# Performance work log

Measured on AMD Instinct MI355X. Metric: run time of the kernel, lower is better.

Reference implementation:

```python
import jax, jax.numpy as jnp
import numpy as np

B, T, X, H, Z, Y, G = 4096, 32, 256, 256, 128, 2, 128


def setup_inputs() -> dict:
    key = jax.random.key(0)
    ks = jax.random.split(key, 16)
    rn = lambda k, s, sc=0.05: jax.random.normal(k, s, dtype=jnp.float32) * sc
    n_days = jnp.concatenate([jnp.array([T], dtype=jnp.int32),
                              jax.random.randint(ks[2], (B - 1,), 1, T + 1).astype(jnp.int32)])
    return {
        "x": rn(ks[0], (B, T, X), 1.0),
        "y_true": jax.nn.softmax(jax.random.normal(ks[1], (B, T, Y), dtype=jnp.float32), axis=-1),
        "n_days": n_days,
        "z0": rn(ks[3], (B, Z), 1.0),
        "eps": rn(ks[4], (T, B, Z), 1.0),
        "W_ih": rn(ks[5], (3 * H, X)), "W_hh": rn(ks[6], (3 * H, H)),
        "b_ih": jnp.zeros((3 * H,), jnp.float32), "b_hh": jnp.zeros((3 * H,), jnp.float32),
        "Wph": rn(ks[7], (Z, X + H + Z)), "bph": jnp.zeros((Z,), jnp.float32),
        "Woh": rn(ks[8], (Z, X + H + Y + Z)), "boh": jnp.zeros((Z,), jnp.float32),
        "Wpm": rn(ks[9], (Z, Z)), "bpm": jnp.zeros((Z,), jnp.float32),
        "Wps": rn(ks[10], (Z, Z)), "bps": jnp.zeros((Z,), jnp.float32),
        "Wqm": rn(ks[11], (Z, Z)), "bqm": jnp.zeros((Z,), jnp.float32),
        "Wqs": rn(ks[12], (Z, Z)), "bqs": jnp.zeros((Z,), jnp.float32),
        "Wg": rn(ks[13], (G, H + Z)), "bg": jnp.zeros((G,), jnp.float32),
        "Wy": rn(ks[14], (Y, G)), "by": jnp.zeros((Y,), jnp.float32),
    }


def _forward(x, y_true, z0, eps, W_ih, W_hh, b_ih, b_hh, Wph, bph, Woh, boh,
             Wpm, bpm, Wps, bps, Wqm, bqm, Wqs, bqs, Wg, bg, Wy, by, n_days):
    xt = jnp.transpose(x, (1, 0, 2))       # [T, B, X]
    yt = jnp.transpose(y_true, (1, 0, 2))  # [T, B, Y]

    # --- GRU over time (torch nn.GRU gate math) ---
    def gru_step(h, xi):
        gi = xi @ W_ih.T + b_ih
        gh = h @ W_hh.T + b_hh
        ir, iz, inn = jnp.split(gi, 3, axis=-1)
        hr, hz, hn = jnp.split(gh, 3, axis=-1)
        r = jax.nn.sigmoid(ir + hr)
        u = jax.nn.sigmoid(iz + hz)
        n = jnp.tanh(inn + r * hn)
        h_new = (1.0 - u) * n + u * h
        return h_new, h_new

    h0 = jnp.zeros((x.shape[0], H), x.dtype)
    _, hs = jax.lax.scan(gru_step, h0, xt)  # [T, B, H]
    # pack/pad semantics: padded timesteps produce zero outputs
    valid = jnp.arange(T)[:, None] < n_days[None, :]  # [T, B]
    hs = jnp.where(valid[:, :, None], hs, 0.0)

    # --- sequential VAE latent scan: z_t depends on z_{t-1} ---
    def vmd_step(z, inputs):
        xi, hi, yi, ei = inputs
        hzp = jnp.tanh(jnp.concatenate([xi, hi, z], -1) @ Wph.T + bph)
        mp = hzp @ Wpm.T + bpm
        sp = jnp.sqrt(jnp.exp(hzp @ Wps.T + bps))
        hzq = jnp.tanh(jnp.concatenate([xi, hi, yi, z], -1) @ Woh.T + boh)
        mq = hzq @ Wqm.T + bqm
        sq = jnp.sqrt(jnp.exp(hzq @ Wqs.T + bqs))
        z_post = mq + sq * ei
        # kl_normal_normal(post || prior)
        kl = jnp.log(sp / sq) + (sq * sq + (mq - mp) ** 2) / (2.0 * sp * sp) - 0.5
        return z_post, (z_post, kl)

    _, (z_posts, kls_e) = jax.lax.scan(vmd_step, z0, (xt, hs, yt, eps))
    kls = jnp.sum(kls_e, axis=-1).T  # [B, T]

    hz = jnp.concatenate([jnp.transpose(hs, (1, 0, 2)),
                          jnp.transpose(z_posts, (1, 0, 2))], -1)  # [B, T, H+Z]
    g = jnp.tanh(hz @ Wg.T + bg)                     # [B, T, G]
    y_pred = jax.nn.softmax(g @ Wy.T + by, axis=-1)  # [B, T, Y]

    idx = n_days - 1
    b = jnp.arange(x.shape[0])
    g_T = g[b, idx]       # [B, G]
    y_T = y_pred[b, idx]  # [B, Y]
    return jnp.concatenate([g_T, y_T, kls], axis=-1)  # [B, G+Y+T]


def reference(x, y_true, n_days, z0, eps, W_ih, W_hh, b_ih, b_hh, Wph, bph,
              Woh, boh, Wpm, bpm, Wps, bps, Wqm, bqm, Wqs, bqs, Wg, bg, Wy, by):
    return _forward(x, y_true, z0, eps, W_ih, W_hh, b_ih, b_hh, Wph, bph, Woh,
                    boh, Wpm, bpm, Wps, bps, Wqm, bqm, Wqs, bqs, Wg, bg, Wy, by,
                    n_days)
```

## Files before the change

kernel.cpp:

```cpp
#include <hip/hip_runtime.h>

typedef unsigned short u16;
typedef short bf16x8 __attribute__((ext_vector_type(8)));
typedef float f32x4 __attribute__((ext_vector_type(4)));

__device__ __forceinline__ float bf2f(u16 v){
  union { unsigned u; float f; } x; x.u = ((unsigned)v) << 16; return x.f;
}
__device__ __forceinline__ u16 f2bf(float f){
  union { float f; unsigned u; } x; x.f = f;
  unsigned u = x.u;
  u += 0x7fffu + ((u >> 16) & 1u);
  return (u16)(u >> 16);
}
__device__ __forceinline__ unsigned pk_bf16(float lo, float hi){
  unsigned r;
  asm("v_cvt_pk_bf16_f32 %0, %1, %2" : "=v"(r) : "v"(lo), "v"(hi));
  return r;
}
__device__ __forceinline__ u16 el4(ushort4 v, int r){ return r==0?v.x:r==1?v.y:r==2?v.z:v.w; }
__device__ __forceinline__ float elf4(float4 v, int r){ return r==0?v.x:r==1?v.y:r==2?v.z:v.w; }
__device__ __forceinline__ float sigm(float x){ return 1.f/(1.f+__expf(-x)); }
__device__ __forceinline__ float tanh_s(float x){ return 1.f - 2.f/(__expf(2.f*x)+1.f); }
__device__ __forceinline__ f32x4 mfma16(bf16x8 a, bf16x8 b, f32x4 c){
  return __builtin_amdgcn_mfma_f32_16x16x32_bf16(a, b, c, 0, 0, 0);
}
__device__ __forceinline__ void gl2lds16(const void* g, void* l){
  __builtin_amdgcn_global_load_lds(
      (const __attribute__((address_space(1))) unsigned int*)g,
      (__attribute__((address_space(3))) unsigned int*)l, 16, 0, 0);
}

__global__ void prep_w(const float* __restrict__ W_ih, const float* __restrict__ W_hh,
                       const float* __restrict__ Wph, const float* __restrict__ Woh,
                       const float* __restrict__ Wpm, const float* __restrict__ Wps,
                       const float* __restrict__ Wqm, const float* __restrict__ Wqs,
                       const float* __restrict__ Wg,  const float* __restrict__ bph,
                       const float* __restrict__ boh,
                       u16* __restrict__ wsb, float* __restrict__ Woy, float* __restrict__ bpq)
{
  int idx = blockIdx.x*256 + threadIdx.x;
  if (idx < 196608){ wsb[idx] = f2bf(W_ih[idx]); return; }
  if (idx < 393216){ wsb[idx] = f2bf(W_hh[idx-196608]); return; }
  if (idx < 524288){ int j = idx-393216; int row = j>>9, col = j&511;
    float v = (row<128) ? Wph[row*640+col] : Woh[(row-128)*642+col];
    wsb[idx] = f2bf(v); return; }
  if (idx < 540672){ int j = idx-524288; int row=j>>7, col=j&127; wsb[idx]=f2bf(Wph[row*640+512+col]); return; }
  if (idx < 557056){ int j = idx-540672; int row=j>>7, col=j&127; wsb[idx]=f2bf(Woh[row*642+514+col]); return; }
  if (idx < 573440){ wsb[idx]=f2bf(Wpm[idx-557056]); return; }
  if (idx < 589824){ wsb[idx]=f2bf(Wps[idx-573440]); return; }
  if (idx < 606208){ wsb[idx]=f2bf(Wqm[idx-589824]); return; }
  if (idx < 622592){ wsb[idx]=f2bf(Wqs[idx-606208]); return; }
  if (idx < 671744){ wsb[idx]=f2bf(Wg[idx-622592]); return; }
  if (idx < 672000){ int j = idx-671744; int row=j>>1; Woy[j] = Woh[row*642+512+(j&1)]; return; }
  if (idx < 672256){ int j = idx-672000; bpq[j] = (j<128) ? bph[j] : boh[j-128]; return; }
}

__global__ void prep_b(const float* __restrict__ b_ih, const float* __restrict__ b_hh,
                       float* __restrict__ bsum)
{
  int j = threadIdx.x;
  if (j < 768) bsum[j] = b_ih[j] + (j < 512 ? b_hh[j] : 0.f);
}

__global__ void prep_x(const float* __restrict__ x, u16* __restrict__ xbf){
  int i = blockIdx.x*256 + threadIdx.x;
  if (i >= 4194304) return;
  const float4* src = (const float4*)(x + (size_t)i*8);
  float4 a = src[0], b = src[1];
  uint4 o;
  o.x = pk_bf16(a.x, a.y);
  o.y = pk_bf16(a.z, a.w);
  o.z = pk_bf16(b.x, b.y);
  o.w = pk_bf16(b.z, b.w);
  ((uint4*)xbf)[i] = o;
}

__global__ void sort_days(const int* __restrict__ n_days, int* __restrict__ perm,
                          int* __restrict__ nd_s, int* __restrict__ cnt)
{
  __shared__ int hist[34];
  __shared__ int base[34];
  __shared__ int cursor[34];
  int tid = threadIdx.x;
  if (tid < 34) hist[tid] = 0;
  __syncthreads();
  for (int i = tid; i < 4096; i += 1024) atomicAdd(&hist[n_days[i]], 1);
  __syncthreads();
  if (tid == 0){
    int acc = 0;
    for (int v = 32; v >= 1; --v){ base[v] = acc; acc += hist[v]; }
    base[0] = acc;
  }
  __syncthreads();
  if (tid < 33) cursor[tid] = base[tid];
  if (tid < 32) cnt[tid] = base[tid];
  __syncthreads();
  for (int i = tid; i < 4096; i += 1024){
    int v = n_days[i];
    int pos = atomicAdd(&cursor[v], 1);
    perm[pos] = i;
    nd_s[pos] = v;
  }
}

__global__ __launch_bounds__(512, 4) void gemm_gi(
  const u16* __restrict__ A, const u16* __restrict__ W,
  const float* __restrict__ bias, const int* __restrict__ perm,
  const int* __restrict__ cnt, u16* __restrict__ C)
{
  const int t  = blockIdx.x >> 5;
  const int rt = blockIdx.x & 31;
  if (rt*128 >= cnt[t]) return;
  const int n0 = blockIdx.y*256;
  const int tid = threadIdx.x;
  const int w = tid>>6, lane = tid&63, c = lane&15, g = lane>>4;
  const int wm = w>>2, wn = w&3;
  __shared__ __align__(16) char smem[49152];
  u16* abuf = (u16*)smem;
  u16* wbuf = (u16*)(smem + 16384);
  u16* clds = (u16*)smem;

  size_t asrc[2];
  #pragma unroll
  for (int i=0;i<2;++i){
    int p = (w*2+i)*64 + lane;
    int k8 = p>>7, row = p&127;
    asrc[i] = ((size_t)perm[rt*128 + row]*32 + t)*256 + k8*8;
  }
  size_t wsrc[4];
  #pragma unroll
  for (int i=0;i<4;++i){
    int p = (w*4+i)*64 + lane;
    int k8 = p>>8, row = p&255;
    wsrc[i] = (size_t)(n0+row)*256 + k8*8;
  }
  f32x4 acc[4][4];
  #pragma unroll
  for (int i=0;i<4;++i)
    #pragma unroll
    for (int j=0;j<4;++j) acc[i][j] = (f32x4){0.f,0.f,0.f,0.f};
  for (int kc=0; kc<4; ++kc){
    __syncthreads();
    #pragma unroll
    for (int i=0;i<2;++i) gl2lds16(A + asrc[i] + kc*64, &abuf[(w*2+i)*512]);
    #pragma unroll
    for (int i=0;i<4;++i) gl2lds16(W + wsrc[i] + kc*64, &wbuf[(w*4+i)*512]);
    __syncthreads();
    #pragma unroll
    for (int ks=0;ks<2;++ks){
      int k8 = ks*4 + g;
      bf16x8 a[4];
      #pragma unroll
      for (int mt=0;mt<4;++mt) a[mt] = *(const bf16x8*)&abuf[(k8*128 + wm*64 + mt*16 + c)*8];
      #pragma unroll
      for (int nt=0;nt<4;++nt){
        bf16x8 b = *(const bf16x8*)&wbuf[(k8*256 + wn*64 + nt*16 + c)*8];
        #pragma unroll
        for (int mt=0;mt<4;++mt)
          acc[mt][nt] = mfma16(a[mt], b, acc[mt][nt]);
      }
    }
  }
  __syncthreads();
  const size_t crow = (size_t)t*4096 + rt*128;
  #pragma unroll
  for (int nh=0; nh<2; ++nh){
    if ((wn>>1) == nh){
      #pragma unroll
      for (int nt=0;nt<4;++nt){
        int n = n0 + wn*64 + nt*16 + c;
        float bn = bias[n];
        int lc = (wn&1)*64 + nt*16 + c;
        #pragma unroll
        for (int mt=0;mt<4;++mt){
          int lr = wm*64 + mt*16 + g*4;
          #pragma unroll
          for (int r=0;r<4;++r)
            clds[(lr+r)*136 + lc] = f2bf(acc[mt][nt][r] + bn);
        }
      }
    }
    __syncthreads();
    #pragma unroll
    for (int p=0;p<4;++p){
      int idx = p*512 + tid;
      int row = idx>>4, ch = idx&15;
      *(uint4*)(C + (crow+row)*768 + n0 + nh*128 + ch*8)
        = *(const uint4*)&clds[row*136 + ch*8];
    }
    __syncthreads();
  }
}

__global__ __launch_bounds__(512, 4) void gemm_hpq(
  const u16* __restrict__ A1, const u16* __restrict__ A2,
  const u16* __restrict__ W, const float* __restrict__ bias,
  const float* __restrict__ yt, const float* __restrict__ Woy,
  u16* __restrict__ C)
{
  const int m0 = blockIdx.x*128;
  const int tid = threadIdx.x;
  const int w = tid>>6, lane = tid&63, c = lane&15, g = lane>>4;
  const int wm = w>>2, wn = w&3;
  __shared__ __align__(16) char smem[49152];
  u16* abuf = (u16*)smem;
  u16* wbuf = (u16*)(smem + 16384);
  u16* clds = (u16*)smem;

  size_t asrc[2];
  #pragma unroll
  for (int i=0;i<2;++i){
    int p = (w*2+i)*64 + lane;
    int k8 = p>>7, row = p&127;
    asrc[i] = (size_t)(m0+row)*256 + k8*8;
  }
  size_t wsrc[4];
  #pragma unroll
  for (int i=0;i<4;++i){
    int p = (w*4+i)*64 + lane;
    int k8 = p>>8, row = p&255;
    wsrc[i] = (size_t)row*512 + k8*8;
  }
  f32x4 acc[4][4];
  #pragma unroll
  for (int i=0;i<4;++i)
    #pragma unroll
    for (int j=0;j<4;++j) acc[i][j] = (f32x4){0.f,0.f,0.f,0.f};
  for (int kc=0; kc<8; ++kc){
    __syncthreads();
    const u16* Ab = (kc < 4) ? A1 : A2;
    int ko = (kc & 3)*64;
    #pragma unroll
    for (int i=0;i<2;++i) gl2lds16(Ab + asrc[i] + ko, &abuf[(w*2+i)*512]);
    #pragma unroll
    for (int i=0;i<4;++i) gl2lds16(W + wsrc[i] + kc*64, &wbuf[(w*4+i)*512]);
    __syncthreads();
    #pragma unroll
    for (int ks=0;ks<2;++ks){
      int k8 = ks*4 + g;
      bf16x8 a[4];
      #pragma unroll
      for (int mt=0;mt<4;++mt) a[mt] = *(const bf16x8*)&abuf[(k8*128 + wm*64 + mt*16 + c)*8];
      #pragma unroll
      for (int nt=0;nt<4;++nt){
        bf16x8 b = *(const bf16x8*)&wbuf[(k8*256 + wn*64 + nt*16 + c)*8];
        #pragma unroll
        for (int mt=0;mt<4;++mt)
          acc[mt][nt] = mfma16(a[mt], b, acc[mt][nt]);
      }
    }
  }
  __syncthreads();
  #pragma unroll
  for (int nh=0; nh<2; ++nh){
    if ((wn>>1) == nh){
      #pragma unroll
      for (int nt=0;nt<4;++nt){
        int n = wn*64 + nt*16 + c;
        float bn = bias[n];
        float wy0 = 0.f, wy1 = 0.f;
        bool yfl = (n >= 128);
        if (yfl){ wy0 = Woy[(n-128)*2]; wy1 = Woy[(n-128)*2+1]; }
        int lc = (wn&1)*64 + nt*16 + c;
        #pragma unroll
        for (int mt=0;mt<4;++mt){
          int lr = wm*64 + mt*16 + g*4;
          #pragma unroll
          for (int r=0;r<4;++r){
            size_t m = (size_t)m0 + lr + r;
            float v = acc[mt][nt][r] + bn;
            if (yfl) v += yt[2*m]*wy0 + yt[2*m+1]*wy1;
            clds[(lr+r)*136 + lc] = f2bf(v);
          }
        }
      }
    }
    __syncthreads();
    #pragma unroll
    for (int p=0;p<4;++p){
      int idx = p*512 + tid;
      int row = idx>>4, ch = idx&15;
      *(uint4*)(C + (size_t)(m0+row)*256 + nh*128 + ch*8)
        = *(const uint4*)&clds[row*136 + ch*8];
    }
    __syncthreads();
  }
}

__global__ __launch_bounds__(1024, 4) void gru_seq(
  const u16* __restrict__ GI, const u16* __restrict__ Whh,
  const float* __restrict__ bhh, const int* __restrict__ perm,
  const int* __restrict__ nd_s, u16* __restrict__ hs)
{
  const int b0 = blockIdx.x*16;
  const int tid = threadIdx.x;
  const int w = tid>>6, lane = tid&63, c = lane&15, g = lane>>4;
  const int j0 = w*16 + g*4;
  __shared__ __align__(16) u16 hbuf[2][4096];
  __shared__ __align__(16) u16 gibuf[5][12288];

  bf16x8 wa[3][8];
  #pragma unroll
  for (int gate=0; gate<3; ++gate)
    #pragma unroll
    for (int ks=0; ks<8; ++ks)
      wa[gate][ks] = *(const bf16x8*)&Whh[(size_t)(gate*256 + w*16 + c)*256 + ks*32 + g*8];

  const float4 bhn4 = *(const float4*)(bhh + 512 + j0);
  const int ndc   = nd_s[b0 + c];
  const int bound = nd_s[b0];
  const int ob    = perm[b0 + c];

  int so0, so1;
  { int pe = w*512 + lane*8; int row = pe/768, off = pe - row*768;
    so0 = (b0+row)*768 + (off ^ ((row&7)<<3)); }
  { int pe = (16+w)*512 + lane*8; int row = pe/768, off = pe - row*768;
    so1 = (b0+row)*768 + (off ^ ((row&7)<<3)); }
  const int rd0 = c*1536 + ((j0*2) ^ ((c&7)<<4));
  const int hroff = (g*16 + c)*16;
  const int hwoff = ((w*2 + (g>>1))*16 + c)*16 + (g&1)*8;
  u16* hsp = hs + (size_t)ob*8192 + j0;

  float hprev[4] = {0.f,0.f,0.f,0.f};
  if (tid < 512) ((uint4*)hbuf[0])[tid] = make_uint4(0,0,0,0);

  const size_t PL = 3145728;
  #pragma unroll
  for (int p=0; p<4; ++p){
    int pp = (p < bound) ? p : bound-1;
    gl2lds16(GI + (size_t)pp*PL + so0, (char*)gibuf[p] + w*1024);
    if (w < 8) gl2lds16(GI + (size_t)pp*PL + so1, (char*)gibuf[p] + (16+w)*1024);
  }
  asm volatile("s_waitcnt vmcnt(0)" ::: "memory");
  __syncthreads();

  const u16* hr = hbuf[0];
  u16*       hw = hbuf[1];
  int cur = 0;
  #pragma unroll 1
  for (int t=0; t<bound; ++t){
    if (w < 8) asm volatile("s_waitcnt vmcnt(9)" ::: "memory");
    else       asm volatile("s_waitcnt vmcnt(6)" ::: "memory");
    __builtin_amdgcn_sched_barrier(0);
    const char* gib = (const char*)gibuf[cur];
    ushort4 gr_ = *(const ushort4*)(gib + rd0);
    ushort4 gu_ = *(const ushort4*)(gib + rd0 + 512);
    ushort4 gn_ = *(const ushort4*)(gib + rd0 + 1024);
    f32x4 aR = (f32x4){0.f,0.f,0.f,0.f};
    f32x4 aU = (f32x4){0.f,0.f,0.f,0.f};
    f32x4 aN = (f32x4){bhn4.x, bhn4.y, bhn4.z, bhn4.w};
    __builtin_amdgcn_s_setprio(1);
    #pragma unroll
    for (int ks=0; ks<8; ++ks){
      bf16x8 hf = *(const bf16x8*)((const char*)hr + hroff + ks*1024);
      aR = mfma16(wa[0][ks], hf, aR);
      aU = mfma16(wa[1][ks], hf, aU);
      aN = mfma16(wa[2][ks], hf, aN);
    }
    __builtin_amdgcn_s_setprio(0);
    {
      float h4[4];
      #pragma unroll
      for (int r=0; r<4; ++r){
        float rr = sigm(bf2f(el4(gr_,r)) + aR[r]);
        float uu = sigm(bf2f(el4(gu_,r)) + aU[r]);
        float nn = tanh_s(bf2f(el4(gn_,r)) + rr*aN[r]);
        float h = nn + uu*(hprev[r]-nn);
        hprev[r] = h;
        h4[r] = h;
      }
      uint2 hpk;
      hpk.x = pk_bf16(h4[0], h4[1]);
      hpk.y = pk_bf16(h4[2], h4[3]);
      *(uint2*)((char*)hw + hwoff) = hpk;
      uint2 hst = (t < ndc) ? hpk : make_uint2(0u,0u);
      *(uint2*)(hsp + t*256) = hst;
    }
    __builtin_amdgcn_sched_barrier(0);
    {
      int pf = (t+4 < bound) ? t+4 : bound-1;
      int nxt = cur;
      nxt = cur >= 1 ? cur-1 : 4;
      gl2lds16(GI + (size_t)pf*PL + so0, (char*)gibuf[nxt] + w*1024);
      if (w < 8) gl2lds16(GI + (size_t)pf*PL + so1, (char*)gibuf[nxt] + (16+w)*1024);
    }
    asm volatile("s_waitcnt lgkmcnt(0)" ::: "memory");
    __builtin_amdgcn_sched_barrier(0);
    __builtin_amdgcn_s_barrier();
    __builtin_amdgcn_sched_barrier(0);
    { const u16* tmp = hr; hr = hw; hw = (u16*)tmp; }
    cur = (cur == 4) ? 0 : cur+1;
  }
  for (int t2 = bound; t2 < 32; ++t2)
    *(uint2*)(hsp + t2*256) = make_uint2(0u,0u);
}

__global__ __launch_bounds__(512) void vae_seq(
  const u16* __restrict__ HPQ, const float* __restrict__ z0,
  const float* __restrict__ eps, const int* __restrict__ n_days,
  const u16* __restrict__ Wm,
  const float* __restrict__ bpm, const float* __restrict__ bps,
  const float* __restrict__ bqm, const float* __restrict__ bqs,
  u16* __restrict__ zidx, float* __restrict__ out)
{
  const int b0 = blockIdx.x*16;
  const int tid = threadIdx.x, w = tid>>6, lane = tid&63, c = lane&15;
  const int g2 = lane>>4;
  const int j0 = w*16 + g2*4;
  __shared__ __align__(16) u16 zbuf[16*16*8];
  __shared__ __align__(16) u16 hzpb[16*16*8];
  __shared__ __align__(16) u16 hzqb[16*16*8];
  __shared__ float klb[32][16][8];

  bf16x8 wf[6][4];
  #pragma unroll
  for (int mat=0;mat<6;++mat)
    #pragma unroll
    for (int ks=0;ks<4;++ks)
      wf[mat][ks] = *(const bf16x8*)&Wm[mat*16384 + (w*16+c)*128 + ks*32 + g2*8];

  const float4 bpm4 = *(const float4*)(bpm + j0);
  const float4 bps4 = *(const float4*)(bps + j0);
  const float4 bqm4 = *(const float4*)(bqm + j0);
  const float4 bqs4 = *(const float4*)(bqs + j0);
  const int ndc = n_days[b0 + c];

  const int hroff = (g2*16 + c)*16;
  const int hwoff = ((w*2 + (g2>>1))*16 + c)*16 + (g2&1)*8;
  const u16*  hbp = HPQ + ((size_t)(b0+c)*32)*256 + j0;
  const float* ebp = eps + (size_t)(b0+c)*128 + j0;

  if (tid < 256){
    int k8 = tid>>4, row = tid&15;
    const float* zp = z0 + (size_t)(b0+row)*128 + k8*8;
    uint4 o;
    o.x = pk_bf16(zp[0], zp[1]);
    o.y = pk_bf16(zp[2], zp[3]);
    o.z = pk_bf16(zp[4], zp[5]);
    o.w = pk_bf16(zp[6], zp[7]);
    ((uint4*)zbuf)[tid] = o;
  }
  __syncthreads();

  ushort4 pA = *(const ushort4*)(hbp);
  ushort4 qA = *(const ushort4*)(hbp + 128);
  float4  eA = *(const float4*)(ebp);
  ushort4 pB = *(const ushort4*)(hbp + 256);
  ushort4 qB = *(const ushort4*)(hbp + 384);
  float4  eB = *(const float4*)(ebp + 524288);

  uint2 zsel = make_uint2(0u,0u);

  auto step = [&](ushort4& hp4, ushort4& hq4, float4& e4, int t){
    f32x4 accP = (f32x4){0,0,0,0}, accQ = (f32x4){0,0,0,0};
    #pragma unroll
    for (int ks=0;ks<4;++ks){
      bf16x8 zf = *(const bf16x8*)((const char*)zbuf + hroff + ks*1024);
      accP = mfma16(wf[0][ks], zf, accP);
      accQ = mfma16(wf[1][ks], zf, accQ);
    }
    float p4[4], q4[4];
    #pragma unroll
    for (int r=0;r<4;++r){
      p4[r] = tanh_s(bf2f(el4(hp4,r)) + accP[r]);
      q4[r] = tanh_s(bf2f(el4(hq4,r)) + accQ[r]);
    }
    uint2 ppk, qpk;
    ppk.x = pk_bf16(p4[0], p4[1]);  ppk.y = pk_bf16(p4[2], p4[3]);
    qpk.x = pk_bf16(q4[0], q4[1]);  qpk.y = pk_bf16(q4[2], q4[3]);
    *(uint2*)((char*)hzpb + hwoff) = ppk;
    *(uint2*)((char*)hzqb + hwoff) = qpk;
    asm volatile("s_waitcnt lgkmcnt(0)" ::: "memory");
    __builtin_amdgcn_sched_barrier(0);
    __builtin_amdgcn_s_barrier();
    __builtin_amdgcn_sched_barrier(0);
    f32x4 aMP=(f32x4){0,0,0,0}, aAP=(f32x4){0,0,0,0};
    f32x4 aMQ=(f32x4){0,0,0,0}, aAQ=(f32x4){0,0,0,0};
    #pragma unroll
    for (int ks=0;ks<4;++ks){
      bf16x8 pf = *(const bf16x8*)((const char*)hzpb + hroff + ks*1024);
      bf16x8 qf = *(const bf16x8*)((const char*)hzqb + hroff + ks*1024);
      aMP = mfma16(wf[2][ks], pf, aMP);
      aAP = mfma16(wf[3][ks], pf, aAP);
      aMQ = mfma16(wf[4][ks], qf, aMQ);
      aAQ = mfma16(wf[5][ks], qf, aAQ);
    }
    float kls = 0.f;
    float z4[4];
    #pragma unroll
    for (int r=0;r<4;++r){
      float mp = aMP[r]+elf4(bpm4,r);
      float ap = aAP[r]+elf4(bps4,r);
      float mq = aMQ[r]+elf4(bqm4,r);
      float aq = aAQ[r]+elf4(bqs4,r);
      float ev = elf4(e4,r);
      float z = mq + __expf(0.5f*aq)*ev;
      float d = mq - mp;
      kls += 0.5f*(ap-aq) + 0.5f*(__expf(aq)+d*d)*__expf(-ap) - 0.5f;
      z4[r] = z;
    }
    uint2 zpk;
    zpk.x = pk_bf16(z4[0], z4[1]);
    zpk.y = pk_bf16(z4[2], z4[3]);
    *(uint2*)((char*)zbuf + hwoff) = zpk;
    if (t == ndc-1) zsel = zpk;
    kls += __shfl_xor(kls, 16);
    kls += __shfl_xor(kls, 32);
    if (lane < 16) klb[t][c][w] = kls;
    if (t < 30){
      hp4 = *(const ushort4*)(hbp + (t+2)*256);
      hq4 = *(const ushort4*)(hbp + (t+2)*256 + 128);
      e4  = *(const float4*)(ebp + (size_t)(t+2)*524288);
    }
    asm volatile("s_waitcnt lgkmcnt(0)" ::: "memory");
    __builtin_amdgcn_sched_barrier(0);
    __builtin_amdgcn_s_barrier();
    __builtin_amdgcn_sched_barrier(0);
  };

  #pragma unroll 1
  for (int t=0; t<32; t+=2){
    step(pA, qA, eA, t);
    step(pB, qB, eB, t+1);
  }

  *(uint2*)(zidx + (size_t)(b0+c)*128 + j0) = zsel;
  {
    int t2 = tid>>4, c2 = tid&15;
    float s = 0.f;
    #pragma unroll
    for (int ww=0;ww<8;++ww) s += klb[t2][c2][ww];
    out[(size_t)(b0+c2)*162 + 130 + t2] = s;
  }
}

__global__ __launch_bounds__(128) void head_k(
  const u16* __restrict__ hs, const u16* __restrict__ zidx,
  const int* __restrict__ n_days, const u16* __restrict__ Wgb,
  const float* __restrict__ bg, const float* __restrict__ Wy,
  const float* __restrict__ by, float* __restrict__ out)
{
  const int b = blockIdx.x;
  const int tid = threadIdx.x;
  const int lane = tid & 63, wv = tid >> 6;
  __shared__ float hz[384];
  __shared__ float red[2][2];
  const int idx = n_days[b]-1;
  const u16* hrow = hs + ((size_t)b*32 + idx)*256;
  for (int k=tid; k<256; k+=128) hz[k] = bf2f(hrow[k]);
  hz[256+tid] = bf2f(zidx[(size_t)b*128 + tid]);
  __syncthreads();
  const u16* wrow = Wgb + (size_t)tid*384;
  float s = 0.f;
  #pragma unroll 4
  for (int k8=0;k8<48;++k8){
    bf16x8 wvv = *(const bf16x8*)&wrow[k8*8];
    #pragma unroll
    for (int e=0;e<8;++e) s += bf2f((u16)wvv[e]) * hz[k8*8+e];
  }
  float gv = tanh_s(s + bg[tid]);
  out[(size_t)b*162 + tid] = gv;
  float a0 = gv*Wy[tid], a1 = gv*Wy[128+tid];
  #pragma unroll
  for (int off=1; off<64; off<<=1){
    a0 += __shfl_xor(a0, off);
    a1 += __shfl_xor(a1, off);
  }
  if (lane == 0){ red[0][wv] = a0; red[1][wv] = a1; }
  __syncthreads();
  if (tid == 0){
    float l0 = by[0] + red[0][0] + red[0][1];
    float l1 = by[1] + red[1][0] + red[1][1];
    float mx = fmaxf(l0,l1);
    float e0 = __expf(l0-mx), e1 = __expf(l1-mx);
    float si = e0+e1;
    out[(size_t)b*162 + 128] = e0/si;
    out[(size_t)b*162 + 129] = e1/si;
  }
}

extern "C" void kernel_launch(void* const* d_in, const int* in_sizes, int n_in,
                              void* d_out, int out_size, void* d_ws, size_t ws_size,
                              hipStream_t stream)
{
  const float* x      = (const float*)d_in[0];
  const float* y_true = (const float*)d_in[1];
  const int*   n_days = (const int*)d_in[2];
  const float* z0     = (const float*)d_in[3];
  const float* eps    = (const float*)d_in[4];
  const float* W_ih   = (const float*)d_in[5];
  const float* W_hh   = (const float*)d_in[6];
  const float* b_ih   = (const float*)d_in[7];
  const float* b_hh   = (const float*)d_in[8];
  const float* Wph    = (const float*)d_in[9];
  const float* bph    = (const float*)d_in[10];
  const float* Woh    = (const float*)d_in[11];
  const float* boh    = (const float*)d_in[12];
  const float* Wpm    = (const float*)d_in[13];
  const float* bpm    = (const float*)d_in[14];
  const float* Wps    = (const float*)d_in[15];
  const float* bps    = (const float*)d_in[16];
  const float* Wqm    = (const float*)d_in[17];
  const float* bqm    = (const float*)d_in[18];
  const float* Wqs    = (const float*)d_in[19];
  const float* bqs    = (const float*)d_in[20];
  const float* Wg     = (const float*)d_in[21];
  const float* bg     = (const float*)d_in[22];
  const float* Wy     = (const float*)d_in[23];
  const float* by     = (const float*)d_in[24];
  (void)in_sizes; (void)n_in; (void)out_size; (void)ws_size;

  u16*   wsb = (u16*)d_ws;
  float* wsf = (float*)d_ws;
  int*   wsi = (int*)d_ws;
  u16* Wih_b = wsb + 0;
  u16* Whh_b = wsb + 196608;
  u16* Wc_b  = wsb + 393216;
  u16* Wz_b  = wsb + 524288;
  u16* Wg_b  = wsb + 622592;
  float* Woy  = wsf + 335872;
  float* bpq  = wsf + 336128;
  float* bsum = wsf + 336384;
  int* perm   = wsi + 337152;
  int* nd_s   = wsi + 341248;
  int* cnt    = wsi + 345344;
  u16* xbf   = wsb + 690752;
  u16* GI    = wsb + 34245184;
  u16* hsB   = wsb + 134908480;
  u16* HPQ   = wsb + 168462912;
  u16* zidx  = wsb + 202017344;

  hipLaunchKernelGGL(prep_w, dim3(2626), dim3(256), 0, stream,
                     W_ih, W_hh, Wph, Woh, Wpm, Wps, Wqm, Wqs, Wg, bph, boh,
                     wsb, Woy, bpq);
  hipLaunchKernelGGL(prep_b, dim3(1), dim3(768), 0, stream, b_ih, b_hh, bsum);
  hipLaunchKernelGGL(prep_x, dim3(16384), dim3(256), 0, stream, x, xbf);
  hipLaunchKernelGGL(sort_days, dim3(1), dim3(1024), 0, stream,
                     n_days, perm, nd_s, cnt);
  hipLaunchKernelGGL(gemm_gi, dim3(1024,3), dim3(512), 0, stream,
                     xbf, Wih_b, bsum, perm, cnt, GI);
  hipLaunchKernelGGL(gru_seq, dim3(256), dim3(1024), 0, stream,
                     GI, Whh_b, b_hh, perm, nd_s, hsB);
  hipLaunchKernelGGL(gemm_hpq, dim3(1024), dim3(512), 0, stream,
                     xbf, hsB, Wc_b, bpq, y_true, Woy, HPQ);
  hipLaunchKernelGGL(vae_seq, dim3(256), dim3(512), 0, stream,
                     HPQ, z0, eps, n_days, Wz_b, bpm, bps, bqm, bqs, zidx, (float*)d_out);
  hipLaunchKernelGGL(head_k, dim3(4096), dim3(128), 0, stream,
                     hsB, zidx, n_days, Wg_b, bg, Wy, by, (float*)d_out);
}
```

Baseline: 489.8 us.

## Halve GRU batch tile to 8 rows and launch twice as many blocks

The sequential GRU kernel now gives each block 8 sorted batch rows instead of 16, so 512 blocks launch instead of 256 and the MI355X's compute units are better filled during the latency-bound recurrence. The MFMA still computes 16 columns, but lanes with c>=8 skip the gate math and stores, and the GI prefetch buffers and load mapping are shrunk to match. In exchange, half of each MFMA's work is wasted, the W_hh fragment loads are duplicated across twice as many blocks, and the __launch_bounds__ change to 8 may tighten register limits.

```diff
diff --git a/kernel.cpp b/kernel.cpp
--- a/kernel.cpp
+++ b/kernel.cpp
@@ -288,17 +288,18 @@
   }
 }
 
-__global__ __launch_bounds__(1024, 4) void gru_seq(
+__global__ __launch_bounds__(1024, 8) void gru_seq(
   const u16* __restrict__ GI, const u16* __restrict__ Whh,
   const float* __restrict__ bhh, const int* __restrict__ perm,
   const int* __restrict__ nd_s, u16* __restrict__ hs)
 {
-  const int b0 = blockIdx.x*16;
+  const int b0 = blockIdx.x*8;
   const int tid = threadIdx.x;
   const int w = tid>>6, lane = tid&63, c = lane&15, g = lane>>4;
   const int j0 = w*16 + g*4;
+  const bool act = (c < 8);
   __shared__ __align__(16) u16 hbuf[2][4096];
-  __shared__ __align__(16) u16 gibuf[5][12288];
+  __shared__ __align__(16) u16 gibuf[5][6144];
 
   bf16x8 wa[3][8];
   #pragma unroll
@@ -308,29 +309,28 @@
       wa[gate][ks] = *(const bf16x8*)&Whh[(size_t)(gate*256 + w*16 + c)*256 + ks*32 + g*8];
 
   const float4 bhn4 = *(const float4*)(bhh + 512 + j0);
-  const int ndc   = nd_s[b0 + c];
   const int bound = nd_s[b0];
-  const int ob    = perm[b0 + c];
-
-  int so0, so1;
-  { int pe = w*512 + lane*8; int row = pe/768, off = pe - row*768;
-    so0 = (b0+row)*768 + (off ^ ((row&7)<<3)); }
-  { int pe = (16+w)*512 + lane*8; int row = pe/768, off = pe - row*768;
-    so1 = (b0+row)*768 + (off ^ ((row&7)<<3)); }
+  const int ndc   = act ? nd_s[b0 + c] : 0;
+  const int ob    = act ? perm[b0 + c] : 0;
+
+  int so;
+  { int pe = w*384 + lane*8;
+    int row = pe/768; if (row > 7) row = 7;
+    int off = pe - row*768; if (off > 760) off = 760;
+    so = (b0+row)*768 + (off ^ ((row&7)<<3)); }
   const int rd0 = c*1536 + ((j0*2) ^ ((c&7)<<4));
   const int hroff = (g*16 + c)*16;
   const int hwoff = ((w*2 + (g>>1))*16 + c)*16 + (g&1)*8;
   u16* hsp = hs + (size_t)ob*8192 + j0;
 
   float hprev[4] = {0.f,0.f,0.f,0.f};
-  if (tid < 512) ((uint4*)hbuf[0])[tid] = make_uint4(0,0,0,0);
+  ((uint4*)hbuf)[tid] = make_uint4(0,0,0,0);
 
   const size_t PL = 3145728;
   #pragma unroll
   for (int p=0; p<4; ++p){
     int pp = (p < bound) ? p : bound-1;
-    gl2lds16(GI + (size_t)pp*PL + so0, (char*)gibuf[p] + w*1024);
-    if (w < 8) gl2lds16(GI + (size_t)pp*PL + so1, (char*)gibuf[p] + (16+w)*1024);
+    if (lane < 48) gl2lds16(GI + (size_t)pp*PL + so, (char*)gibuf[p] + w*768);
   }
   asm volatile("s_waitcnt vmcnt(0)" ::: "memory");
   __syncthreads();
@@ -340,13 +340,8 @@
   int cur = 0;
   #pragma unroll 1
   for (int t=0; t<bound; ++t){
-    if (w < 8) asm volatile("s_waitcnt vmcnt(9)" ::: "memory");
-    else       asm volatile("s_waitcnt vmcnt(6)" ::: "memory");
-    __builtin_amdgcn_sched_barrier(0);
-    const char* gib = (const char*)gibuf[cur];
-    ushort4 gr_ = *(const ushort4*)(gib + rd0);
-    ushort4 gu_ = *(const ushort4*)(gib + rd0 + 512);
-    ushort4 gn_ = *(const ushort4*)(gib + rd0 + 1024);
+    asm volatile("s_waitcnt vmcnt(6)" ::: "memory");
+    __builtin_amdgcn_sched_barrier(0);
     f32x4 aR = (f32x4){0.f,0.f,0.f,0.f};
     f32x4 aU = (f32x4){0.f,0.f,0.f,0.f};
     f32x4 aN = (f32x4){bhn4.x, bhn4.y, bhn4.z, bhn4.w};
@@ -359,7 +354,11 @@
       aN = mfma16(wa[2][ks], hf, aN);
     }
     __builtin_amdgcn_s_setprio(0);
-    {
+    if (act){
+      const char* gib = (const char*)gibuf[cur];
+      ushort4 gr_ = *(const ushort4*)(gib + rd0);
+      ushort4 gu_ = *(const ushort4*)(gib + rd0 + 512);
+      ushort4 gn_ = *(const ushort4*)(gib + rd0 + 1024);
       float h4[4];
       #pragma unroll
       for (int r=0; r<4; ++r){
@@ -380,10 +379,8 @@
     __builtin_amdgcn_sched_barrier(0);
     {
       int pf = (t+4 < bound) ? t+4 : bound-1;
-      int nxt = cur;
-      nxt = cur >= 1 ? cur-1 : 4;
-      gl2lds16(GI + (size_t)pf*PL + so0, (char*)gibuf[nxt] + w*1024);
-      if (w < 8) gl2lds16(GI + (size_t)pf*PL + so1, (char*)gibuf[nxt] + (16+w)*1024);
+      int nxt = cur >= 1 ? cur-1 : 4;
+      if (lane < 48) gl2lds16(GI + (size_t)pf*PL + so, (char*)gibuf[nxt] + w*768);
     }
     asm volatile("s_waitcnt lgkmcnt(0)" ::: "memory");
     __builtin_amdgcn_sched_barrier(0);
@@ -392,8 +389,10 @@
     { const u16* tmp = hr; hr = hw; hw = (u16*)tmp; }
     cur = (cur == 4) ? 0 : cur+1;
   }
-  for (int t2 = bound; t2 < 32; ++t2)
-    *(uint2*)(hsp + t2*256) = make_uint2(0u,0u);
+  if (act){
+    for (int t2 = bound; t2 < 32; ++t2)
+      *(uint2*)(hsp + t2*256) = make_uint2(0u,0u);
+  }
 }
 
 __global__ __launch_bounds__(512) void vae_seq(
@@ -640,7 +639,7 @@
                      n_days, perm, nd_s, cnt);
   hipLaunchKernelGGL(gemm_gi, dim3(1024,3), dim3(512), 0, stream,
                      xbf, Wih_b, bsum, perm, cnt, GI);
-  hipLaunchKernelGGL(gru_seq, dim3(256), dim3(1024), 0, stream,
+  hipLaunchKernelGGL(gru_seq, dim3(512), dim3(1024), 0, stream,
                      GI, Whh_b, b_hh, perm, nd_s, hsB);
   hipLaunchKernelGGL(gemm_hpq, dim3(1024), dim3(512), 0, stream,
                      xbf, hsB, Wc_b, bpq, y_true, Woy, HPQ);
```

Result: slower. 897.9 us (+83.3%).

## Halve GRU recurrence block to 8 waves, each computing two column tiles

Applied to the files above, without the earlier changes.

The sequential GRU kernel now runs 512 threads per block instead of 1024. Each wave owns 32 hidden columns (two 16-wide MFMA tiles), so it holds twice the W_hh fragments in registers and issues six MFMAs per k-step. This is meant to cut barrier cost per timestep and make the GI prefetch uniform across waves (three loads each). In exchange it raises register pressure (48 bf16x8 weight vectors per thread) and gives fewer waves to hide latency on the serial critical path.

```diff
diff --git a/kernel.cpp b/kernel.cpp
--- a/kernel.cpp
+++ b/kernel.cpp
@@ -288,7 +288,7 @@
   }
 }
 
-__global__ __launch_bounds__(1024, 4) void gru_seq(
+__global__ __launch_bounds__(512, 2) void gru_seq(
   const u16* __restrict__ GI, const u16* __restrict__ Whh,
   const float* __restrict__ bhh, const int* __restrict__ perm,
   const int* __restrict__ nd_s, u16* __restrict__ hs)
@@ -296,41 +296,54 @@
   const int b0 = blockIdx.x*16;
   const int tid = threadIdx.x;
   const int w = tid>>6, lane = tid&63, c = lane&15, g = lane>>4;
-  const int j0 = w*16 + g*4;
+  const int j0 = w*32 + g*4;
   __shared__ __align__(16) u16 hbuf[2][4096];
   __shared__ __align__(16) u16 gibuf[5][12288];
-
-  bf16x8 wa[3][8];
+  __shared__ float bhnl[256];
+
+  bf16x8 wa[3][2][8];
   #pragma unroll
   for (int gate=0; gate<3; ++gate)
     #pragma unroll
-    for (int ks=0; ks<8; ++ks)
-      wa[gate][ks] = *(const bf16x8*)&Whh[(size_t)(gate*256 + w*16 + c)*256 + ks*32 + g*8];
-
-  const float4 bhn4 = *(const float4*)(bhh + 512 + j0);
+    for (int ct=0; ct<2; ++ct)
+      #pragma unroll
+      for (int ks=0; ks<8; ++ks)
+        wa[gate][ct][ks] = *(const bf16x8*)&Whh[(size_t)(gate*256 + w*32 + ct*16 + c)*256 + ks*32 + g*8];
+
+  if (tid < 256) bhnl[tid] = bhh[512 + tid];
+  const int bound = nd_s[b0];
   const int ndc   = nd_s[b0 + c];
-  const int bound = nd_s[b0];
   const int ob    = perm[b0 + c];
 
-  int so0, so1;
-  { int pe = w*512 + lane*8; int row = pe/768, off = pe - row*768;
-    so0 = (b0+row)*768 + (off ^ ((row&7)<<3)); }
-  { int pe = (16+w)*512 + lane*8; int row = pe/768, off = pe - row*768;
-    so1 = (b0+row)*768 + (off ^ ((row&7)<<3)); }
-  const int rd0 = c*1536 + ((j0*2) ^ ((c&7)<<4));
+  int so[3];
+  #pragma unroll
+  for (int i=0;i<3;++i){
+    int pe = (w*3+i)*512 + lane*8;
+    int row = pe/768, off = pe - row*768;
+    so[i] = (b0+row)*768 + (off ^ ((row&7)<<3));
+  }
+  const int rdA = c*1536 + ((j0*2) ^ ((c&7)<<4));
+  const int rdB = c*1536 + (((j0+16)*2) ^ ((c&7)<<4));
   const int hroff = (g*16 + c)*16;
-  const int hwoff = ((w*2 + (g>>1))*16 + c)*16 + (g&1)*8;
+  const int hwoffA = ((w*4 + (g>>1))*16 + c)*16 + (g&1)*8;
+  const int hwoffB = hwoffA + 512;
   u16* hsp = hs + (size_t)ob*8192 + j0;
 
-  float hprev[4] = {0.f,0.f,0.f,0.f};
-  if (tid < 512) ((uint4*)hbuf[0])[tid] = make_uint4(0,0,0,0);
+  float hprev[2][4];
+  #pragma unroll
+  for (int ct=0;ct<2;++ct)
+    #pragma unroll
+    for (int r=0;r<4;++r) hprev[ct][r] = 0.f;
+  ((uint4*)hbuf)[tid] = make_uint4(0,0,0,0);
+  ((uint4*)hbuf)[tid+512] = make_uint4(0,0,0,0);
 
   const size_t PL = 3145728;
   #pragma unroll
   for (int p=0; p<4; ++p){
     int pp = (p < bound) ? p : bound-1;
-    gl2lds16(GI + (size_t)pp*PL + so0, (char*)gibuf[p] + w*1024);
-    if (w < 8) gl2lds16(GI + (size_t)pp*PL + so1, (char*)gibuf[p] + (16+w)*1024);
+    #pragma unroll
+    for (int i=0;i<3;++i)
+      gl2lds16(GI + (size_t)pp*PL + so[i], (char*)gibuf[p] + (w*3+i)*1024);
   }
   asm volatile("s_waitcnt vmcnt(0)" ::: "memory");
   __syncthreads();
@@ -340,50 +353,62 @@
   int cur = 0;
   #pragma unroll 1
   for (int t=0; t<bound; ++t){
-    if (w < 8) asm volatile("s_waitcnt vmcnt(9)" ::: "memory");
-    else       asm volatile("s_waitcnt vmcnt(6)" ::: "memory");
-    __builtin_amdgcn_sched_barrier(0);
-    const char* gib = (const char*)gibuf[cur];
-    ushort4 gr_ = *(const ushort4*)(gib + rd0);
-    ushort4 gu_ = *(const ushort4*)(gib + rd0 + 512);
-    ushort4 gn_ = *(const ushort4*)(gib + rd0 + 1024);
-    f32x4 aR = (f32x4){0.f,0.f,0.f,0.f};
-    f32x4 aU = (f32x4){0.f,0.f,0.f,0.f};
-    f32x4 aN = (f32x4){bhn4.x, bhn4.y, bhn4.z, bhn4.w};
+    asm volatile("s_waitcnt vmcnt(15)" ::: "memory");
+    __builtin_amdgcn_sched_barrier(0);
+    float4 bhnA = *(const float4*)&bhnl[j0];
+    float4 bhnB = *(const float4*)&bhnl[j0+16];
+    f32x4 aR0=(f32x4){0,0,0,0}, aR1=(f32x4){0,0,0,0};
+    f32x4 aU0=(f32x4){0,0,0,0}, aU1=(f32x4){0,0,0,0};
+    f32x4 aN0=(f32x4){bhnA.x,bhnA.y,bhnA.z,bhnA.w};
+    f32x4 aN1=(f32x4){bhnB.x,bhnB.y,bhnB.z,bhnB.w};
     __builtin_amdgcn_s_setprio(1);
     #pragma unroll
     for (int ks=0; ks<8; ++ks){
       bf16x8 hf = *(const bf16x8*)((const char*)hr + hroff + ks*1024);
-      aR = mfma16(wa[0][ks], hf, aR);
-      aU = mfma16(wa[1][ks], hf, aU);
-      aN = mfma16(wa[2][ks], hf, aN);
+      aR0 = mfma16(wa[0][0][ks], hf, aR0);
+      aR1 = mfma16(wa[0][1][ks], hf, aR1);
+      aU0 = mfma16(wa[1][0][ks], hf, aU0);
+      aU1 = mfma16(wa[1][1][ks], hf, aU1);
+      aN0 = mfma16(wa[2][0][ks], hf, aN0);
+      aN1 = mfma16(wa[2][1][ks], hf, aN1);
     }
     __builtin_amdgcn_s_setprio(0);
     {
-      float h4[4];
-      #pragma unroll
-      for (int r=0; r<4; ++r){
-        float rr = sigm(bf2f(el4(gr_,r)) + aR[r]);
-        float uu = sigm(bf2f(el4(gu_,r)) + aU[r]);
-        float nn = tanh_s(bf2f(el4(gn_,r)) + rr*aN[r]);
-        float h = nn + uu*(hprev[r]-nn);
-        hprev[r] = h;
-        h4[r] = h;
+      const char* gib = (const char*)gibuf[cur];
+      #pragma unroll
+      for (int ct=0; ct<2; ++ct){
+        int rd = ct ? rdB : rdA;
+        ushort4 gr_ = *(const ushort4*)(gib + rd);
+        ushort4 gu_ = *(const ushort4*)(gib + rd + 512);
+        ushort4 gn_ = *(const ushort4*)(gib + rd + 1024);
+        f32x4 aR = ct ? aR1 : aR0;
+        f32x4 aU = ct ? aU1 : aU0;
+        f32x4 aN = ct ? aN1 : aN0;
+        float h4[4];
+        #pragma unroll
+        for (int r=0; r<4; ++r){
+          float rr = sigm(bf2f(el4(gr_,r)) + aR[r]);
+          float uu = sigm(bf2f(el4(gu_,r)) + aU[r]);
+          float nn = tanh_s(bf2f(el4(gn_,r)) + rr*aN[r]);
+          float h = nn + uu*(hprev[ct][r]-nn);
+          hprev[ct][r] = h;
+          h4[r] = h;
+        }
+        uint2 hpk;
+        hpk.x = pk_bf16(h4[0], h4[1]);
+        hpk.y = pk_bf16(h4[2], h4[3]);
+        *(uint2*)((char*)hw + (ct ? hwoffB : hwoffA)) = hpk;
+        uint2 hst = (t < ndc) ? hpk : make_uint2(0u,0u);
+        *(uint2*)(hsp + t*256 + ct*16) = hst;
       }
-      uint2 hpk;
-      hpk.x = pk_bf16(h4[0], h4[1]);
-      hpk.y = pk_bf16(h4[2], h4[3]);
-      *(uint2*)((char*)hw + hwoff) = hpk;
-      uint2 hst = (t < ndc) ? hpk : make_uint2(0u,0u);
-      *(uint2*)(hsp + t*256) = hst;
     }
     __builtin_amdgcn_sched_barrier(0);
     {
       int pf = (t+4 < bound) ? t+4 : bound-1;
-      int nxt = cur;
-      nxt = cur >= 1 ? cur-1 : 4;
-      gl2lds16(GI + (size_t)pf*PL + so0, (char*)gibuf[nxt] + w*1024);
-      if (w < 8) gl2lds16(GI + (size_t)pf*PL + so1, (char*)gibuf[nxt] + (16+w)*1024);
+      int nxt = cur >= 1 ? cur-1 : 4;
+      #pragma unroll
+      for (int i=0;i<3;++i)
+        gl2lds16(GI + (size_t)pf*PL + so[i], (char*)gibuf[nxt] + (w*3+i)*1024);
     }
     asm volatile("s_waitcnt lgkmcnt(0)" ::: "memory");
     __builtin_amdgcn_sched_barrier(0);
@@ -392,8 +417,10 @@
     { const u16* tmp = hr; hr = hw; hw = (u16*)tmp; }
     cur = (cur == 4) ? 0 : cur+1;
   }
-  for (int t2 = bound; t2 < 32; ++t2)
+  for (int t2 = bound; t2 < 32; ++t2){
     *(uint2*)(hsp + t2*256) = make_uint2(0u,0u);
+    *(uint2*)(hsp + t2*256 + 16) = make_uint2(0u,0u);
+  }
 }
 
 __global__ __launch_bounds__(512) void vae_seq(
@@ -640,7 +667,7 @@
                      n_days, perm, nd_s, cnt);
   hipLaunchKernelGGL(gemm_gi, dim3(1024,3), dim3(512), 0, stream,
                      xbf, Wih_b, bsum, perm, cnt, GI);
-  hipLaunchKernelGGL(gru_seq, dim3(256), dim3(1024), 0, stream,
+  hipLaunchKernelGGL(gru_seq, dim3(256), dim3(512), 0, stream,
                      GI, Whh_b, b_hh, perm, nd_s, hsB);
   hipLaunchKernelGGL(gemm_hpq, dim3(1024), dim3(512), 0, stream,
                      xbf, hsB, Wc_b, bpq, y_true, Woy, HPQ);
```

Result: slower. 507.6 us (+3.6%).

## Rewrite head kernel to batch 16 rows per block using MFMA

Applied to the files above, without the earlier changes.

The output head kernel now handles 16 batch rows per 512-thread block. It stages the selected hidden and latent rows in LDS and computes the Wg projection with bf16 MFMA instructions instead of a per-thread scalar dot product. The Wy logits are then reduced with shuffles, softmaxed, and the g and y outputs are written out cooperatively. This cuts block count and scalar FMA work for a small tail kernel, at the cost of more LDS staging and barriers.

```diff
diff --git a/kernel.cpp b/kernel.cpp
--- a/kernel.cpp
+++ b/kernel.cpp
@@ -380,8 +380,7 @@
     __builtin_amdgcn_sched_barrier(0);
     {
       int pf = (t+4 < bound) ? t+4 : bound-1;
-      int nxt = cur;
-      nxt = cur >= 1 ? cur-1 : 4;
+      int nxt = cur >= 1 ? cur-1 : 4;
       gl2lds16(GI + (size_t)pf*PL + so0, (char*)gibuf[nxt] + w*1024);
       if (w < 8) gl2lds16(GI + (size_t)pf*PL + so1, (char*)gibuf[nxt] + (16+w)*1024);
     }
@@ -535,48 +534,78 @@
   }
 }
 
-__global__ __launch_bounds__(128) void head_k(
+__global__ __launch_bounds__(512) void head_k(
   const u16* __restrict__ hs, const u16* __restrict__ zidx,
   const int* __restrict__ n_days, const u16* __restrict__ Wgb,
   const float* __restrict__ bg, const float* __restrict__ Wy,
   const float* __restrict__ by, float* __restrict__ out)
 {
-  const int b = blockIdx.x;
+  const int b0 = blockIdx.x*16;
   const int tid = threadIdx.x;
-  const int lane = tid & 63, wv = tid >> 6;
-  __shared__ float hz[384];
-  __shared__ float red[2][2];
-  const int idx = n_days[b]-1;
-  const u16* hrow = hs + ((size_t)b*32 + idx)*256;
-  for (int k=tid; k<256; k+=128) hz[k] = bf2f(hrow[k]);
-  hz[256+tid] = bf2f(zidx[(size_t)b*128 + tid]);
-  __syncthreads();
-  const u16* wrow = Wgb + (size_t)tid*384;
-  float s = 0.f;
-  #pragma unroll 4
-  for (int k8=0;k8<48;++k8){
-    bf16x8 wvv = *(const bf16x8*)&wrow[k8*8];
-    #pragma unroll
-    for (int e=0;e<8;++e) s += bf2f((u16)wvv[e]) * hz[k8*8+e];
-  }
-  float gv = tanh_s(s + bg[tid]);
-  out[(size_t)b*162 + tid] = gv;
-  float a0 = gv*Wy[tid], a1 = gv*Wy[128+tid];
-  #pragma unroll
-  for (int off=1; off<64; off<<=1){
-    a0 += __shfl_xor(a0, off);
-    a1 += __shfl_xor(a1, off);
-  }
-  if (lane == 0){ red[0][wv] = a0; red[1][wv] = a1; }
-  __syncthreads();
-  if (tid == 0){
-    float l0 = by[0] + red[0][0] + red[0][1];
-    float l1 = by[1] + red[1][0] + red[1][1];
-    float mx = fmaxf(l0,l1);
-    float e0 = __expf(l0-mx), e1 = __expf(l1-mx);
-    float si = e0+e1;
-    out[(size_t)b*162 + 128] = e0/si;
-    out[(size_t)b*162 + 129] = e1/si;
+  const int w = tid>>6, lane = tid&63, c = lane&15, g = lane>>4;
+  __shared__ __align__(16) u16 hzlds[48*16*8];
+  __shared__ float glds[16*128];
+  __shared__ float ylds[16][2];
+
+  for (int i=tid; i<768; i+=512){
+    int row = i & 15, k8 = i >> 4;
+    int b = b0 + row;
+    uint4 v;
+    if (k8 < 32){
+      int idx = n_days[b] - 1;
+      v = *(const uint4*)(hs + ((size_t)b*32 + idx)*256 + k8*8);
+    } else {
+      v = *(const uint4*)(zidx + (size_t)b*128 + (k8-32)*8);
+    }
+    *(uint4*)&hzlds[((size_t)k8*16 + row)*8] = v;
+  }
+  bf16x8 wf[12];
+  #pragma unroll
+  for (int ks=0;ks<12;++ks)
+    wf[ks] = *(const bf16x8*)&Wgb[(size_t)(w*16 + c)*384 + ks*32 + g*8];
+  const float4 bg4 = *(const float4*)(bg + w*16 + g*4);
+  __syncthreads();
+
+  f32x4 acc = (f32x4){0.f,0.f,0.f,0.f};
+  #pragma unroll
+  for (int ks=0;ks<12;++ks){
+    bf16x8 hzf = *(const bf16x8*)&hzlds[((ks*4+g)*16 + c)*8];
+    acc = mfma16(wf[ks], hzf, acc);
+  }
+  #pragma unroll
+  for (int r=0;r<4;++r){
+    float gv = tanh_s(acc[r] + elf4(bg4,r));
+    glds[c*128 + w*16 + g*4 + r] = gv;
+  }
+  __syncthreads();
+  {
+    int row = w*2 + (lane>>5);
+    int ll = lane & 31;
+    float s0 = 0.f, s1 = 0.f;
+    #pragma unroll
+    for (int e=0;e<4;++e){
+      float gv = glds[row*128 + ll*4 + e];
+      s0 += gv * Wy[ll*4+e];
+      s1 += gv * Wy[128 + ll*4+e];
+    }
+    s0 += __shfl_xor(s0,1); s0 += __shfl_xor(s0,2); s0 += __shfl_xor(s0,4);
+    s0 += __shfl_xor(s0,8); s0 += __shfl_xor(s0,16);
+    s1 += __shfl_xor(s1,1); s1 += __shfl_xor(s1,2); s1 += __shfl_xor(s1,4);
+    s1 += __shfl_xor(s1,8); s1 += __shfl_xor(s1,16);
+    if (ll == 0){
+      float l0 = by[0] + s0, l1 = by[1] + s1;
+      float mx = fmaxf(l0,l1);
+      float e0 = __expf(l0-mx), e1 = __expf(l1-mx);
+      float si = e0+e1;
+      ylds[row][0] = e0/si;
+      ylds[row][1] = e1/si;
+    }
+  }
+  __syncthreads();
+  for (int i=tid; i<2080; i+=512){
+    int row = i/130, col = i - row*130;
+    float v = (col < 128) ? glds[row*128 + col] : ylds[row][col-128];
+    out[(size_t)(b0+row)*162 + col] = v;
   }
 }
 
@@ -646,6 +675,6 @@
                      xbf, hsB, Wc_b, bpq, y_true, Woy, HPQ);
   hipLaunchKernelGGL(vae_seq, dim3(256), dim3(512), 0, stream,
                      HPQ, z0, eps, n_days, Wz_b, bpm, bps, bqm, bqs, zidx, (float*)d_out);
-  hipLaunchKernelGGL(head_k, dim3(4096), dim3(128), 0, stream,
+  hipLaunchKernelGGL(head_k, dim3(256), dim3(512), 0, stream,
                      hsB, zidx, n_days, Wg_b, bg, Wy, by, (float*)d_out);
 }
```

Measured after the change: 453.4 us. 1.08x faster.
